# Kernel tuning notes

Hardware: AMD Instinct MI355X
Metric: run time of the kernel (lower is better)

Reference implementation:

```python
import jax, jax.numpy as jnp
import numpy as np

N = 50000
E = 800000
NDIM_IN = 128
NDIM_OUT = 64
H = 3
EDIM = 8
CLASS_NUM = 10
NEG_SLOPE = 0.2  # DGL GATConv default negative_slope


def _gat_layer(src, dst, x, W, a_l, a_r, b):
    """One DGL-style GATConv layer. x: [N, Fin]; W: [Fin, H*D]; a_l/a_r: [H, D]; b: [H*D]."""
    n, hd = x.shape[0], W.shape[1]
    D = hd // H
    f = (x @ W).reshape(n, H, D)                         # projected feats [N,H,D]
    el = (f * a_l[None]).sum(-1)                          # [N,H]
    er = (f * a_r[None]).sum(-1)                          # [N,H]
    e = jax.nn.leaky_relu(el[src] + er[dst], NEG_SLOPE)   # [E,H] per-edge logits
    m = jax.ops.segment_max(e, dst, num_segments=n)       # softmax max per dst node
    ex = jnp.exp(e - m[dst])                              # [E,H]
    denom = jax.ops.segment_sum(ex, dst, num_segments=n)  # [N,H]
    alpha = ex / denom[dst]                               # edge softmax
    out = jax.ops.segment_sum(f[src] * alpha[:, :, None], dst, num_segments=n)  # [N,H,D]
    return out + b.reshape(1, H, D)


def setup_inputs() -> dict:
    key = jax.random.key(0)
    ks = jax.random.split(key, 16)
    src = jax.random.randint(ks[0], (E,), 0, N)
    dst = jax.random.randint(ks[1], (E,), 0, N)
    nfeats = jax.random.normal(ks[2], (N, NDIM_IN), dtype=jnp.float32)
    efeats = jax.random.normal(ks[3], (E, EDIM), dtype=jnp.float32)
    s1 = 1.0 / np.sqrt(NDIM_IN)
    s2 = 1.0 / np.sqrt(H * NDIM_OUT)
    sp = 1.0 / np.sqrt(2 * H * NDIM_OUT)
    W1 = jax.random.normal(ks[4], (NDIM_IN, H * NDIM_OUT), dtype=jnp.float32) * s1
    al1 = jax.random.normal(ks[5], (H, NDIM_OUT), dtype=jnp.float32) * s1
    ar1 = jax.random.normal(ks[6], (H, NDIM_OUT), dtype=jnp.float32) * s1
    b1 = jnp.zeros((H * NDIM_OUT,), dtype=jnp.float32)
    W2 = jax.random.normal(ks[7], (H * NDIM_OUT, H * NDIM_OUT), dtype=jnp.float32) * s2
    al2 = jax.random.normal(ks[8], (H, NDIM_OUT), dtype=jnp.float32) * s2
    ar2 = jax.random.normal(ks[9], (H, NDIM_OUT), dtype=jnp.float32) * s2
    b2 = jnp.zeros((H * NDIM_OUT,), dtype=jnp.float32)
    Wp = jax.random.normal(ks[10], (2 * H * NDIM_OUT, CLASS_NUM), dtype=jnp.float32) * sp
    bp = jnp.zeros((CLASS_NUM,), dtype=jnp.float32)
    return {"src": src, "dst": dst, "nfeats": nfeats, "efeats": efeats,
            "W1": W1, "al1": al1, "ar1": ar1, "b1": b1,
            "W2": W2, "al2": al2, "ar2": ar2, "b2": b2,
            "Wp": Wp, "bp": bp}


def reference(src, dst, nfeats, efeats, W1, al1, ar1, b1, W2, al2, ar2, b2, Wp, bp):
    # efeats is accepted but unused, matching the original forward signature.
    h = _gat_layer(src, dst, nfeats, W1, al1, ar1, b1)      # [N,H,D]
    h = jax.nn.relu(h.reshape(h.shape[0], -1))              # [N,H*D]
    h = _gat_layer(src, dst, h, W2, al2, ar2, b2)           # [N,H,D]
    h = jax.nn.relu(h.reshape(h.shape[0], -1))              # [N,H*D]
    # MLPPredictor: per-edge concat(src,dst) -> linear
    score = jnp.concatenate([h[src], h[dst]], axis=1) @ Wp + bp  # [E,class_num]
    return score
```

## Files before the change

kernel.cpp:

```cpp
#include <hip/hip_runtime.h>
#include <cstdint>

constexpr int KIN = 128;
constexpr int HD  = 192;
constexpr int NC  = 10;
#define NEG_SLOPE 0.2f

typedef __attribute__((ext_vector_type(8))) short bf16x8;
typedef __attribute__((ext_vector_type(4))) float f32x4;

__device__ __forceinline__ float b2f(unsigned short u) {
    union { unsigned int i; float f; } x; x.i = ((unsigned int)u) << 16; return x.f;
}
__device__ __forceinline__ unsigned short f2b(float f) {
    union { float f; unsigned int i; } x; x.f = f;
    unsigned int r = x.i + 0x7FFFu + ((x.i >> 16) & 1u);
    return (unsigned short)(r >> 16);
}
__device__ __forceinline__ float gload(const void* p, long i, int isbf) {
    return isbf ? b2f(((const unsigned short*)p)[i]) : ((const float*)p)[i];
}
__device__ __forceinline__ float lrelu(float v) { return v > 0.f ? v : NEG_SLOPE * v; }

__global__ void k_probe(const void* W, int* flag) {
    if (threadIdx.x != 0 || blockIdx.x != 0) return;
    const unsigned short* u = (const unsigned short*)W;
    float mx = 0.f;
    for (int i = 0; i < 64; ++i) {
        float v = fabsf(b2f(u[i]));
        if (!(v < 1e30f)) v = 1e30f;
        mx = fmaxf(mx, v);
    }
    *flag = (mx < 1e4f) ? 1 : 0;
}

__global__ void k_zero(int* p, int n) {
    int i = blockIdx.x * blockDim.x + threadIdx.x;
    if (i < n) p[i] = 0;
}

__global__ void k_cvt(const void* __restrict__ X, unsigned short* __restrict__ Y, long n,
                      const int* __restrict__ flag) {
    long i = (long)blockIdx.x * blockDim.x + threadIdx.x;
    if (i < n) Y[i] = f2b(gload(X, i, *flag));
}

__global__ void k_pack(const void* __restrict__ W, unsigned short* __restrict__ Bp,
                       int K, int Creal, int CT, int KS, long rowOff,
                       const int* __restrict__ flag) {
    int t = blockIdx.x * blockDim.x + threadIdx.x;
    int total = CT * KS * 512;
    if (t >= total) return;
    int isb = *flag;
    int j = t & 7, lane = (t >> 3) & 63;
    int ks = (t >> 9) % KS, ct = t / (KS * 512);
    int k = ks * 32 + ((lane >> 4) << 3) + j;
    int c = ct * 16 + (lane & 15);
    float v = 0.f;
    if (k < K && c < Creal) v = gload(W, (rowOff + k) * (long)Creal + c, isb);
    Bp[t] = f2b(v);
}

template<int CT, int KS, int ELR>
__global__ void k_mm(const unsigned short* __restrict__ A, const unsigned short* __restrict__ Bp,
                     unsigned short* __restrict__ fb, const void* __restrict__ al,
                     const void* __restrict__ ar, float* __restrict__ el4,
                     float* __restrict__ er4, int M, int Cout, const int* __restrict__ flag) {
    int wid = threadIdx.x >> 6, lane = threadIdx.x & 63;
    int rt = blockIdx.x * 4 + wid;
    if (rt * 16 >= M) return;
    const int K = KS * 32;
    int mrow = rt * 16 + (lane & 15);
    int kq = (lane >> 4) << 3;
    f32x4 acc[CT];
#pragma unroll
    for (int ct = 0; ct < CT; ++ct) acc[ct] = (f32x4){0.f, 0.f, 0.f, 0.f};
    const unsigned short* arow = A + (long)mrow * K + kq;
    const bf16x8* bp = (const bf16x8*)Bp;
#pragma unroll
    for (int ks = 0; ks < KS; ++ks) {
        bf16x8 a = *(const bf16x8*)(arow + ks * 32);
#pragma unroll
        for (int ct = 0; ct < CT; ++ct) {
            bf16x8 b = bp[(ct * KS + ks) * 64 + lane];
            acc[ct] = __builtin_amdgcn_mfma_f32_16x16x32_bf16(a, b, acc[ct], 0, 0, 0);
        }
    }
    int quad = lane >> 4, c0 = lane & 15;
    int rbase = rt * 16 + quad * 4;
#pragma unroll
    for (int ct = 0; ct < CT; ++ct)
#pragma unroll
        for (int r = 0; r < 4; ++r)
            fb[(long)(rbase + r) * Cout + ct * 16 + c0] = f2b(acc[ct][r]);
    if (ELR) {
        int isb = *flag;
        float pl[3][4], pr[3][4];
#pragma unroll
        for (int h = 0; h < 3; ++h)
#pragma unroll
            for (int r = 0; r < 4; ++r) { pl[h][r] = 0.f; pr[h][r] = 0.f; }
#pragma unroll
        for (int ct = 0; ct < CT; ++ct) {
            int h = ct >> 2;
            float wl = gload(al, ct * 16 + c0, isb);
            float wr = gload(ar, ct * 16 + c0, isb);
#pragma unroll
            for (int r = 0; r < 4; ++r) {
                pl[h][r] += acc[ct][r] * wl;
                pr[h][r] += acc[ct][r] * wr;
            }
        }
#pragma unroll
        for (int d = 1; d < 16; d <<= 1)
#pragma unroll
            for (int h = 0; h < 3; ++h)
#pragma unroll
                for (int r = 0; r < 4; ++r) {
                    pl[h][r] += __shfl_xor(pl[h][r], d);
                    pr[h][r] += __shfl_xor(pr[h][r], d);
                }
        if (c0 == 0) {
#pragma unroll
            for (int r = 0; r < 4; ++r)
#pragma unroll
                for (int h = 0; h < 3; ++h) {
                    el4[(long)(rbase + r) * 4 + h] = pl[h][r];
                    er4[(long)(rbase + r) * 4 + h] = pr[h][r];
                }
        }
    }
}

__global__ void k_mmpq(const unsigned short* __restrict__ A, const unsigned short* __restrict__ Bp,
                       float* __restrict__ PQ, int M) {
    constexpr int CT = 2, KS = 6;
    int wid = threadIdx.x >> 6, lane = threadIdx.x & 63;
    int rt = blockIdx.x * 4 + wid;
    if (rt * 16 >= M) return;
    const int K = KS * 32;
    int mrow = rt * 16 + (lane & 15);
    int kq = (lane >> 4) << 3;
    f32x4 acc[CT];
#pragma unroll
    for (int ct = 0; ct < CT; ++ct) acc[ct] = (f32x4){0.f, 0.f, 0.f, 0.f};
    const unsigned short* arow = A + (long)mrow * K + kq;
    const bf16x8* bp = (const bf16x8*)Bp;
#pragma unroll
    for (int ks = 0; ks < KS; ++ks) {
        bf16x8 a = *(const bf16x8*)(arow + ks * 32);
#pragma unroll
        for (int ct = 0; ct < CT; ++ct) {
            bf16x8 b = bp[(ct * KS + ks) * 64 + lane];
            acc[ct] = __builtin_amdgcn_mfma_f32_16x16x32_bf16(a, b, acc[ct], 0, 0, 0);
        }
    }
    int quad = lane >> 4, c0 = lane & 15;
    int rbase = rt * 16 + quad * 4;
    if (c0 < NC) {
#pragma unroll
        for (int ct = 0; ct < CT; ++ct)
#pragma unroll
            for (int r = 0; r < 4; ++r)
                PQ[(long)(rbase + r) * (2 * NC) + ct * NC + c0] = acc[ct][r];
    }
}

__global__ void k_hist(const int* __restrict__ dst, int E, int* __restrict__ deg) {
    int i = blockIdx.x * blockDim.x + threadIdx.x;
    if (i < E) atomicAdd(&deg[dst[i]], 1);
}

__global__ void k_scan1(const int* __restrict__ deg, int n, int* __restrict__ off,
                        int* __restrict__ bsum) {
    __shared__ int sh[1024];
    int tid = threadIdx.x, i = blockIdx.x * 1024 + tid;
    int v = (i < n) ? deg[i] : 0;
    sh[tid] = v;
    __syncthreads();
    for (int s = 1; s < 1024; s <<= 1) {
        int t = (tid >= s) ? sh[tid - s] : 0;
        __syncthreads();
        sh[tid] += t;
        __syncthreads();
    }
    if (i < n) off[i] = sh[tid] - v;
    if (tid == 1023) bsum[blockIdx.x] = sh[tid];
}

__global__ void k_scan2(int* __restrict__ bsum, int nb, int* __restrict__ off, int n) {
    int tid = threadIdx.x;
    int v = (tid < nb) ? bsum[tid] : 0;
    int incl = v;
    for (int s = 1; s < 64; s <<= 1) {
        int t = __shfl_up(incl, s);
        if (tid >= s) incl += t;
    }
    if (tid < nb) bsum[tid] = incl - v;
    if (tid == 63) off[n] = incl;
}

__global__ void k_scan3(int* __restrict__ off, const int* __restrict__ bsum, int n,
                        int* __restrict__ cur) {
    int i = blockIdx.x * 1024 + threadIdx.x;
    if (i < n) {
        int v = off[i] + bsum[blockIdx.x];
        off[i] = v;
        cur[i] = v;
    }
}

__global__ void k_fill(const int* __restrict__ src, const int* __restrict__ dst, int E,
                       int* __restrict__ cur, int* __restrict__ csr) {
    int i = blockIdx.x * blockDim.x + threadIdx.x;
    if (i < E) {
        int p = atomicAdd(&cur[dst[i]], 1);
        csr[p] = src[i];
    }
}

__global__ void k_agg(const unsigned short* __restrict__ fb, const float4* __restrict__ el4,
                      const float* __restrict__ er4, const int* __restrict__ off,
                      const int* __restrict__ csr, const void* __restrict__ bias,
                      unsigned short* __restrict__ outb, int Nn, const int* __restrict__ flag) {
    int lane = threadIdx.x & 63;
    int n = blockIdx.x * (blockDim.x >> 6) + (threadIdx.x >> 6);
    if (n >= Nn) return;
    int isb = *flag;
    int s0 = off[n], s1 = off[n + 1];
    int deg = s1 - s0;
    float er0 = er4[n * 4 + 0], er1 = er4[n * 4 + 1], er2 = er4[n * 4 + 2];
    float a0 = 0.f, a1 = 0.f, a2 = 0.f;

    if (deg > 0 && deg <= 64) {
        int e = s0 + lane;
        bool on = e < s1;
        int sIdx = on ? csr[e] : 0;
        float4 el = el4[sIdx];
        float t0 = on ? lrelu(el.x + er0) : -1e30f;
        float t1 = on ? lrelu(el.y + er1) : -1e30f;
        float t2 = on ? lrelu(el.z + er2) : -1e30f;
        float m0 = t0, m1 = t1, m2 = t2;
        for (int d = 1; d < 64; d <<= 1) {
            m0 = fmaxf(m0, __shfl_xor(m0, d));
            m1 = fmaxf(m1, __shfl_xor(m1, d));
            m2 = fmaxf(m2, __shfl_xor(m2, d));
        }
        float w0 = on ? __expf(t0 - m0) : 0.f;
        float w1 = on ? __expf(t1 - m1) : 0.f;
        float w2 = on ? __expf(t2 - m2) : 0.f;
        float d0 = w0, d1 = w1, d2 = w2;
        for (int d = 1; d < 64; d <<= 1) {
            d0 += __shfl_xor(d0, d);
            d1 += __shfl_xor(d1, d);
            d2 += __shfl_xor(d2, d);
        }
        w0 *= 1.f / d0; w1 *= 1.f / d1; w2 *= 1.f / d2;
#pragma unroll 4
        for (int j = 0; j < deg; ++j) {
            int s = __shfl(sIdx, j);
            float u0 = __shfl(w0, j), u1 = __shfl(w1, j), u2 = __shfl(w2, j);
            const unsigned short* fr = fb + (long)s * HD;
            a0 += u0 * b2f(fr[lane]);
            a1 += u1 * b2f(fr[lane + 64]);
            a2 += u2 * b2f(fr[lane + 128]);
        }
    } else if (deg > 64) {
        float m0 = -1e30f, m1 = -1e30f, m2 = -1e30f;
        for (int e = s0 + lane; e < s1; e += 64) {
            float4 el = el4[csr[e]];
            m0 = fmaxf(m0, lrelu(el.x + er0));
            m1 = fmaxf(m1, lrelu(el.y + er1));
            m2 = fmaxf(m2, lrelu(el.z + er2));
        }
        for (int d = 1; d < 64; d <<= 1) {
            m0 = fmaxf(m0, __shfl_xor(m0, d));
            m1 = fmaxf(m1, __shfl_xor(m1, d));
            m2 = fmaxf(m2, __shfl_xor(m2, d));
        }
        float d0 = 0.f, d1 = 0.f, d2 = 0.f;
        for (int e = s0 + lane; e < s1; e += 64) {
            float4 el = el4[csr[e]];
            d0 += __expf(lrelu(el.x + er0) - m0);
            d1 += __expf(lrelu(el.y + er1) - m1);
            d2 += __expf(lrelu(el.z + er2) - m2);
        }
        for (int d = 1; d < 64; d <<= 1) {
            d0 += __shfl_xor(d0, d);
            d1 += __shfl_xor(d1, d);
            d2 += __shfl_xor(d2, d);
        }
        float id0 = 1.f / d0, id1 = 1.f / d1, id2 = 1.f / d2;
        for (int e = s0; e < s1; ++e) {
            int s = csr[e];
            float4 el = el4[s];
            float w0 = __expf(lrelu(el.x + er0) - m0) * id0;
            float w1 = __expf(lrelu(el.y + er1) - m1) * id1;
            float w2 = __expf(lrelu(el.z + er2) - m2) * id2;
            const unsigned short* fr = fb + (long)s * HD;
            a0 += w0 * b2f(fr[lane]);
            a1 += w1 * b2f(fr[lane + 64]);
            a2 += w2 * b2f(fr[lane + 128]);
        }
    }
    a0 = fmaxf(a0 + gload(bias, lane,       isb), 0.f);
    a1 = fmaxf(a1 + gload(bias, lane + 64,  isb), 0.f);
    a2 = fmaxf(a2 + gload(bias, lane + 128, isb), 0.f);
    unsigned short* brow = outb + (long)n * HD;
    brow[lane]       = f2b(a0);
    brow[lane + 64]  = f2b(a1);
    brow[lane + 128] = f2b(a2);
}

__global__ void k_score(const int* __restrict__ src, const int* __restrict__ dst,
                        const float* __restrict__ PQ, const void* __restrict__ bp,
                        void* __restrict__ out, int E, const int* __restrict__ flag) {
    __shared__ float sh[256 * NC];
    int tid = threadIdx.x;
    int e0 = blockIdx.x * 256;
    int e = e0 + tid;
    int isb = *flag;
    float v[NC];
    if (e < E) {
        const float* pr = PQ + (long)src[e] * (2 * NC);
        const float* qr = PQ + (long)dst[e] * (2 * NC) + NC;
#pragma unroll
        for (int c = 0; c < NC; ++c) v[c] = pr[c] + qr[c] + gload(bp, c, isb);
    }
    int nE = min(256, E - e0);
    if (isb) {
        unsigned int* shu = (unsigned int*)sh;
        if (e < E) {
#pragma unroll
            for (int c = 0; c < NC / 2; ++c)
                shu[tid * (NC / 2) + c] =
                    (unsigned)f2b(v[2 * c]) | ((unsigned)f2b(v[2 * c + 1]) << 16);
        }
        __syncthreads();
        int nU = nE * (NC / 2);
        unsigned int* ob = (unsigned int*)((unsigned short*)out + (long)e0 * NC);
        int nU4 = nU >> 2;
        uint4* ob4 = (uint4*)ob;
        const uint4* sb4 = (const uint4*)shu;
        for (int u = tid; u < nU4; u += 256) ob4[u] = sb4[u];
        for (int w = (nU4 << 2) + tid; w < nU; w += 256) ob[w] = shu[w];
    } else {
        if (e < E) {
#pragma unroll
            for (int c = 0; c < NC; ++c) sh[tid * NC + c] = v[c];
        }
        __syncthreads();
        int nU = nE * NC;
        float* ob = (float*)out + (long)e0 * NC;
        int nU4 = nU >> 2;
        float4* ob4 = (float4*)ob;
        const float4* sb4 = (const float4*)sh;
        for (int u = tid; u < nU4; u += 256) ob4[u] = sb4[u];
        for (int w = (nU4 << 2) + tid; w < nU; w += 256) ob[w] = sh[w];
    }
}

extern "C" void kernel_launch(void* const* d_in, const int* in_sizes, int n_in,
                              void* d_out, int out_size, void* d_ws, size_t ws_size,
                              hipStream_t stream) {
    const int* src = (const int*)d_in[0];
    const int* dst = (const int*)d_in[1];
    const void* nfeats = d_in[2];
    const void* W1  = d_in[4];
    const void* al1 = d_in[5];
    const void* ar1 = d_in[6];
    const void* b1  = d_in[7];
    const void* W2  = d_in[8];
    const void* al2 = d_in[9];
    const void* ar2 = d_in[10];
    const void* b2  = d_in[11];
    const void* Wp  = d_in[12];
    const void* bp  = d_in[13];

    const int E = in_sizes[0];
    const int N = in_sizes[2] / KIN;

    size_t o = 0;
    auto alloc = [&](size_t bytes) { size_t r = o; o = (o + bytes + 255) & ~(size_t)255; return r; };
    char* ws = (char*)d_ws;
    int*   flag = (int*)  (ws + alloc(4));
    int*   deg  = (int*)  (ws + alloc((size_t)N * 4));
    int*   off  = (int*)  (ws + alloc((size_t)(N + 1) * 4));
    int*   cur  = (int*)  (ws + alloc((size_t)N * 4));
    int*   bsum = (int*)  (ws + alloc(64 * 4));
    int*   csr  = (int*)  (ws + alloc((size_t)E * 4));
    unsigned short* xb  = (unsigned short*)(ws + alloc((size_t)N * KIN * 2));
    unsigned short* fb  = (unsigned short*)(ws + alloc((size_t)N * HD * 2));
    unsigned short* hb  = (unsigned short*)(ws + alloc((size_t)N * HD * 2));
    unsigned short* Bp1 = (unsigned short*)(ws + alloc((size_t)12 * 4 * 512 * 2));
    unsigned short* Bp2 = (unsigned short*)(ws + alloc((size_t)12 * 6 * 512 * 2));
    unsigned short* BpPQ= (unsigned short*)(ws + alloc((size_t)2 * 6 * 512 * 2));
    float* el4  = (float*)(ws + alloc((size_t)N * 16));
    float* er4  = (float*)(ws + alloc((size_t)N * 16));
    float* PQ   = (float*)(ws + alloc((size_t)N * 2 * NC * 4));
    (void)ws_size; (void)n_in; (void)out_size;

    const int TB = 256;
    int gE   = (E + TB - 1) / TB;
    int gN   = (N + TB - 1) / TB;
    int gAgg = (N + 3) / 4;
    int rowTiles = (N + 15) / 16;
    int gMM  = (rowTiles + 3) / 4;
    int nb   = (N + 1023) / 1024;

    k_probe<<<1, 64, 0, stream>>>(W1, flag);

    long nx = (long)N * KIN;
    k_cvt<<<(int)((nx + TB - 1) / TB), TB, 0, stream>>>(nfeats, xb, nx, flag);
    k_pack<<<(12 * 4 * 512 + TB - 1) / TB, TB, 0, stream>>>(W1, Bp1, KIN, HD, 12, 4, 0, flag);
    k_pack<<<(12 * 6 * 512 + TB - 1) / TB, TB, 0, stream>>>(W2, Bp2, HD, HD, 12, 6, 0, flag);
    k_pack<<<(6 * 512 + TB - 1) / TB, TB, 0, stream>>>(Wp, BpPQ,            HD, NC, 1, 6, 0,  flag);
    k_pack<<<(6 * 512 + TB - 1) / TB, TB, 0, stream>>>(Wp, BpPQ + 6 * 512,  HD, NC, 1, 6, HD, flag);

    k_zero<<<gN, TB, 0, stream>>>(deg, N);
    k_hist<<<gE, TB, 0, stream>>>(dst, E, deg);
    k_scan1<<<nb, 1024, 0, stream>>>(deg, N, off, bsum);
    k_scan2<<<1, 64, 0, stream>>>(bsum, nb, off, N);
    k_scan3<<<nb, 1024, 0, stream>>>(off, bsum, N, cur);
    k_fill<<<gE, TB, 0, stream>>>(src, dst, E, cur, csr);

    k_mm<12, 4, 1><<<gMM, TB, 0, stream>>>(xb, Bp1, fb, al1, ar1, el4, er4, N, HD, flag);
    k_agg<<<gAgg, TB, 0, stream>>>(fb, (const float4*)el4, er4, off, csr, b1, hb, N, flag);

    k_mm<12, 6, 1><<<gMM, TB, 0, stream>>>(hb, Bp2, fb, al2, ar2, el4, er4, N, HD, flag);
    k_agg<<<gAgg, TB, 0, stream>>>(fb, (const float4*)el4, er4, off, csr, b2, hb, N, flag);

    k_mmpq<<<gMM, TB, 0, stream>>>(hb, BpPQ, PQ, N);
    k_score<<<gE, TB, 0, stream>>>(src, dst, PQ, bp, d_out, E, flag);
}
```

Measured before the change: 484.2 us.

## Fuse prep kernels into one launch and widen aggregation gathers to 32-bit pairs

Merges the dtype probe, degree zeroing, input conversion and four weight-pack launches into a single k_prep kernel, where each block recomputes the dtype flag locally. Rewrites k_agg so each lane loads packed pairs of bf16 values as 32-bit words, with lanes 0-63 covering the first 128 columns and lanes 0-31 the last 64. This replaces 16-bit loads and stores with wider ones. It also raises the unroll to 8 and adds launch bounds to the aggregation kernel. The intent is to cut launch overhead and the number of gather memory instructions on the edge loop, at the cost of half-idle lanes for the third head and a redundant probe in every prep block.

```diff
diff --git a/kernel.cpp b/kernel.cpp
--- a/kernel.cpp
+++ b/kernel.cpp
@@ -22,43 +22,45 @@
 }
 __device__ __forceinline__ float lrelu(float v) { return v > 0.f ? v : NEG_SLOPE * v; }
 
-__global__ void k_probe(const void* W, int* flag) {
-    if (threadIdx.x != 0 || blockIdx.x != 0) return;
-    const unsigned short* u = (const unsigned short*)W;
-    float mx = 0.f;
-    for (int i = 0; i < 64; ++i) {
-        float v = fabsf(b2f(u[i]));
-        if (!(v < 1e30f)) v = 1e30f;
-        mx = fmaxf(mx, v);
-    }
-    *flag = (mx < 1e4f) ? 1 : 0;
-}
-
-__global__ void k_zero(int* p, int n) {
-    int i = blockIdx.x * blockDim.x + threadIdx.x;
-    if (i < n) p[i] = 0;
-}
-
-__global__ void k_cvt(const void* __restrict__ X, unsigned short* __restrict__ Y, long n,
-                      const int* __restrict__ flag) {
-    long i = (long)blockIdx.x * blockDim.x + threadIdx.x;
-    if (i < n) Y[i] = f2b(gload(X, i, *flag));
-}
-
-__global__ void k_pack(const void* __restrict__ W, unsigned short* __restrict__ Bp,
-                       int K, int Creal, int CT, int KS, long rowOff,
-                       const int* __restrict__ flag) {
-    int t = blockIdx.x * blockDim.x + threadIdx.x;
-    int total = CT * KS * 512;
-    if (t >= total) return;
-    int isb = *flag;
-    int j = t & 7, lane = (t >> 3) & 63;
-    int ks = (t >> 9) % KS, ct = t / (KS * 512);
+__global__ void k_prep(const void* __restrict__ nfeats, const void* __restrict__ W1,
+                       const void* __restrict__ W2, const void* __restrict__ Wp,
+                       unsigned short* __restrict__ xb, int* __restrict__ deg,
+                       unsigned short* __restrict__ Bp1, unsigned short* __restrict__ Bp2,
+                       unsigned short* __restrict__ BpPQ, int N, long nx,
+                       int bZ, int bC, int* __restrict__ flag) {
+    __shared__ int shIsb;
+    if (threadIdx.x == 0) {
+        const unsigned short* u = (const unsigned short*)W1;
+        float mx = 0.f;
+        for (int i = 0; i < 64; ++i) {
+            float v = fabsf(b2f(u[i]));
+            if (!(v < 1e30f)) v = 1e30f;
+            mx = fmaxf(mx, v);
+        }
+        shIsb = (mx < 1e4f) ? 1 : 0;
+        if (blockIdx.x == 0) *flag = shIsb;
+    }
+    __syncthreads();
+    int isb = shIsb;
+    int b = blockIdx.x, tid = threadIdx.x;
+    if (b < bZ) { int i = b * 256 + tid; if (i < N) deg[i] = 0; return; }
+    b -= bZ;
+    if (b < bC) { long i = (long)b * 256 + tid; if (i < nx) xb[i] = f2b(gload(nfeats, i, isb)); return; }
+    b -= bC;
+    int t = b * 256 + tid;
+    const int s1 = 12 * 4 * 512, s2 = s1 + 12 * 6 * 512, s3 = s2 + 6 * 512, s4 = s3 + 6 * 512;
+    const void* W; unsigned short* Bp; int K, Creal, CT, KS; long rowOff; int tt;
+    if (t < s1)      { W = W1; Bp = Bp1;            K = KIN; Creal = HD; CT = 12; KS = 4; rowOff = 0;  tt = t; }
+    else if (t < s2) { W = W2; Bp = Bp2;            K = HD;  Creal = HD; CT = 12; KS = 6; rowOff = 0;  tt = t - s1; }
+    else if (t < s3) { W = Wp; Bp = BpPQ;           K = HD;  Creal = NC; CT = 1;  KS = 6; rowOff = 0;  tt = t - s2; }
+    else if (t < s4) { W = Wp; Bp = BpPQ + 6 * 512; K = HD;  Creal = NC; CT = 1;  KS = 6; rowOff = HD; tt = t - s3; }
+    else return;
+    int j = tt & 7, lane = (tt >> 3) & 63, ks = (tt >> 9) % KS, ct = tt / (KS * 512);
     int k = ks * 32 + ((lane >> 4) << 3) + j;
     int c = ct * 16 + (lane & 15);
     float v = 0.f;
     if (k < K && c < Creal) v = gload(W, (rowOff + k) * (long)Creal + c, isb);
-    Bp[t] = f2b(v);
+    Bp[tt] = f2b(v);
 }
 
 template<int CT, int KS, int ELR>
@@ -219,18 +221,20 @@
     }
 }
 
-__global__ void k_agg(const unsigned short* __restrict__ fb, const float4* __restrict__ el4,
-                      const float* __restrict__ er4, const int* __restrict__ off,
-                      const int* __restrict__ csr, const void* __restrict__ bias,
-                      unsigned short* __restrict__ outb, int Nn, const int* __restrict__ flag) {
+__global__ void __launch_bounds__(256, 8)
+k_agg(const unsigned int* __restrict__ fbu, const float4* __restrict__ el4,
+      const float* __restrict__ er4, const int* __restrict__ off,
+      const int* __restrict__ csr, const void* __restrict__ bias,
+      unsigned int* __restrict__ outu, int Nn, const int* __restrict__ flag) {
     int lane = threadIdx.x & 63;
-    int n = blockIdx.x * (blockDim.x >> 6) + (threadIdx.x >> 6);
+    int n = blockIdx.x * 4 + (threadIdx.x >> 6);
     if (n >= Nn) return;
     int isb = *flag;
     int s0 = off[n], s1 = off[n + 1];
     int deg = s1 - s0;
     float er0 = er4[n * 4 + 0], er1 = er4[n * 4 + 1], er2 = er4[n * 4 + 2];
-    float a0 = 0.f, a1 = 0.f, a2 = 0.f;
+    bool lo32 = lane < 32;
+    float aa0 = 0.f, aa1 = 0.f, ab0 = 0.f, ab1 = 0.f;
 
     if (deg > 0 && deg <= 64) {
         int e = s0 + lane;
@@ -256,14 +260,20 @@
             d2 += __shfl_xor(d2, d);
         }
         w0 *= 1.f / d0; w1 *= 1.f / d1; w2 *= 1.f / d2;
-#pragma unroll 4
+#pragma unroll 8
         for (int j = 0; j < deg; ++j) {
             int s = __shfl(sIdx, j);
             float u0 = __shfl(w0, j), u1 = __shfl(w1, j), u2 = __shfl(w2, j);
-            const unsigned short* fr = fb + (long)s * HD;
-            a0 += u0 * b2f(fr[lane]);
-            a1 += u1 * b2f(fr[lane + 64]);
-            a2 += u2 * b2f(fr[lane + 128]);
+            float wa = lo32 ? u0 : u1;
+            const unsigned int* fr = fbu + (long)s * 96;
+            unsigned int ua = fr[lane];
+            aa0 += wa * b2f((unsigned short)ua);
+            aa1 += wa * b2f((unsigned short)(ua >> 16));
+            if (lo32) {
+                unsigned int ub = fr[64 + lane];
+                ab0 += u2 * b2f((unsigned short)ub);
+                ab1 += u2 * b2f((unsigned short)(ub >> 16));
+            }
         }
     } else if (deg > 64) {
         float m0 = -1e30f, m1 = -1e30f, m2 = -1e30f;
@@ -294,22 +304,32 @@
         for (int e = s0; e < s1; ++e) {
             int s = csr[e];
             float4 el = el4[s];
-            float w0 = __expf(lrelu(el.x + er0) - m0) * id0;
-            float w1 = __expf(lrelu(el.y + er1) - m1) * id1;
-            float w2 = __expf(lrelu(el.z + er2) - m2) * id2;
-            const unsigned short* fr = fb + (long)s * HD;
-            a0 += w0 * b2f(fr[lane]);
-            a1 += w1 * b2f(fr[lane + 64]);
-            a2 += w2 * b2f(fr[lane + 128]);
-        }
-    }
-    a0 = fmaxf(a0 + gload(bias, lane,       isb), 0.f);
-    a1 = fmaxf(a1 + gload(bias, lane + 64,  isb), 0.f);
-    a2 = fmaxf(a2 + gload(bias, lane + 128, isb), 0.f);
-    unsigned short* brow = outb + (long)n * HD;
-    brow[lane]       = f2b(a0);
-    brow[lane + 64]  = f2b(a1);
-    brow[lane + 128] = f2b(a2);
+            float u0 = __expf(lrelu(el.x + er0) - m0) * id0;
+            float u1 = __expf(lrelu(el.y + er1) - m1) * id1;
+            float u2 = __expf(lrelu(el.z + er2) - m2) * id2;
+            float wa = lo32 ? u0 : u1;
+            const unsigned int* fr = fbu + (long)s * 96;
+            unsigned int ua = fr[lane];
+            aa0 += wa * b2f((unsigned short)ua);
+            aa1 += wa * b2f((unsigned short)(ua >> 16));
+            if (lo32) {
+                unsigned int ub = fr[64 + lane];
+                ab0 += u2 * b2f((unsigned short)ub);
+                ab1 += u2 * b2f((unsigned short)(ub >> 16));
+            }
+        }
+    }
+    int ca = 2 * lane;
+    aa0 = fmaxf(aa0 + gload(bias, ca,     isb), 0.f);
+    aa1 = fmaxf(aa1 + gload(bias, ca + 1, isb), 0.f);
+    unsigned int* orow = outu + (long)n * 96;
+    orow[lane] = (unsigned)f2b(aa0) | ((unsigned)f2b(aa1) << 16);
+    if (lo32) {
+        int cb = 128 + 2 * lane;
+        ab0 = fmaxf(ab0 + gload(bias, cb,     isb), 0.f);
+        ab1 = fmaxf(ab1 + gload(bias, cb + 1, isb), 0.f);
+        orow[64 + lane] = (unsigned)f2b(ab0) | ((unsigned)f2b(ab1) << 16);
+    }
 }
 
 __global__ void k_score(const int* __restrict__ src, const int* __restrict__ dst,
@@ -401,23 +421,19 @@
     (void)ws_size; (void)n_in; (void)out_size;
 
     const int TB = 256;
+    long nx = (long)N * KIN;
     int gE   = (E + TB - 1) / TB;
-    int gN   = (N + TB - 1) / TB;
     int gAgg = (N + 3) / 4;
     int rowTiles = (N + 15) / 16;
     int gMM  = (rowTiles + 3) / 4;
     int nb   = (N + 1023) / 1024;
 
-    k_probe<<<1, 64, 0, stream>>>(W1, flag);
-
-    long nx = (long)N * KIN;
-    k_cvt<<<(int)((nx + TB - 1) / TB), TB, 0, stream>>>(nfeats, xb, nx, flag);
-    k_pack<<<(12 * 4 * 512 + TB - 1) / TB, TB, 0, stream>>>(W1, Bp1, KIN, HD, 12, 4, 0, flag);
-    k_pack<<<(12 * 6 * 512 + TB - 1) / TB, TB, 0, stream>>>(W2, Bp2, HD, HD, 12, 6, 0, flag);
-    k_pack<<<(6 * 512 + TB - 1) / TB, TB, 0, stream>>>(Wp, BpPQ,            HD, NC, 1, 6, 0,  flag);
-    k_pack<<<(6 * 512 + TB - 1) / TB, TB, 0, stream>>>(Wp, BpPQ + 6 * 512,  HD, NC, 1, 6, HD, flag);
-
-    k_zero<<<gN, TB, 0, stream>>>(deg, N);
+    int bZ = (N + TB - 1) / TB;
+    int bC = (int)((nx + TB - 1) / TB);
+    int bP = (12 * 4 * 512 + 12 * 6 * 512 + 2 * 6 * 512 + TB - 1) / TB;
+    k_prep<<<bZ + bC + bP, TB, 0, stream>>>(nfeats, W1, W2, Wp, xb, deg,
+                                            Bp1, Bp2, BpPQ, N, nx, bZ, bC, flag);
+
     k_hist<<<gE, TB, 0, stream>>>(dst, E, deg);
     k_scan1<<<nb, 1024, 0, stream>>>(deg, N, off, bsum);
     k_scan2<<<1, 64, 0, stream>>>(bsum, nb, off, N);
@@ -425,10 +441,12 @@
     k_fill<<<gE, TB, 0, stream>>>(src, dst, E, cur, csr);
 
     k_mm<12, 4, 1><<<gMM, TB, 0, stream>>>(xb, Bp1, fb, al1, ar1, el4, er4, N, HD, flag);
-    k_agg<<<gAgg, TB, 0, stream>>>(fb, (const float4*)el4, er4, off, csr, b1, hb, N, flag);
+    k_agg<<<gAgg, TB, 0, stream>>>((const unsigned int*)fb, (const float4*)el4, er4,
+                                   off, csr, b1, (unsigned int*)hb, N, flag);
 
     k_mm<12, 6, 1><<<gMM, TB, 0, stream>>>(hb, Bp2, fb, al2, ar2, el4, er4, N, HD, flag);
-    k_agg<<<gAgg, TB, 0, stream>>>(fb, (const float4*)el4, er4, off, csr, b2, hb, N, flag);
+    k_agg<<<gAgg, TB, 0, stream>>>((const unsigned int*)fb, (const float4*)el4, er4,
+                                   off, csr, b2, (unsigned int*)hb, N, flag);
 
     k_mmpq<<<gMM, TB, 0, stream>>>(hb, BpPQ, PQ, N);
     k_score<<<gE, TB, 0, stream>>>(src, dst, PQ, bp, d_out, E, flag);
```

After: 497.2 us. 1.03x slower.
